# Optimization experiments

Hardware: AMD Instinct MI355X
Metric: run time of the kernel (lower is better)

The kernel has to match this reference:

```python
import jax, jax.numpy as jnp
import numpy as np

N = 50000      # num nodes
C_IN = 128     # channels[0]
C_OUT = 128    # channels[1]
D = 16         # fixed node degree
T = 4          # diffusion steps
H_MLP = 64     # diff_mlp hidden
H_GRU = 128    # GRUAggr hidden
EPS = 0.01


def setup_inputs() -> dict:
    key = jax.random.key(0)
    ks = jax.random.split(key, 10)
    node_attr = jax.random.normal(ks[0], (N, C_IN), jnp.float32)
    # adjacency sorted by source: node i owns columns [i*D, i*D+D)
    src = jnp.repeat(jnp.arange(N), D)
    dst = jax.random.randint(ks[1], (N * D,), 0, N)
    edge_index = jnp.stack([src, dst])                       # [2, N*D]
    slices = jnp.stack([jnp.arange(N) * D, jnp.full((N,), D)], axis=1)  # [N,2] (start,count)
    noise = EPS * jax.random.normal(ks[2], (T, N, D), jnp.float32)      # eps*randn per step
    init = lambda k, shape, fan: (jax.random.normal(k, shape, jnp.float32) / np.sqrt(fan))
    W1 = init(ks[3], ((1 + T) * C_IN, H_MLP), (1 + T) * C_IN)
    b1 = jnp.zeros((H_MLP,), jnp.float32)
    W2 = init(ks[4], (H_MLP, 1), H_MLP)
    b2 = jnp.zeros((1,), jnp.float32)
    Wx = init(ks[5], (C_IN, 3 * H_GRU), C_IN)
    Wh = init(ks[6], (H_GRU, 3 * H_GRU), H_GRU)
    bx = jnp.zeros((3 * H_GRU,), jnp.float32)
    bh = jnp.zeros((3 * H_GRU,), jnp.float32)
    Wo = init(ks[7], (H_GRU, C_OUT), H_GRU)
    bo = jnp.zeros((C_OUT,), jnp.float32)
    return dict(node_attr=node_attr, edge_index=edge_index, slices=slices, noise=noise,
                W1=W1, b1=b1, W2=W2, b2=b2, Wx=Wx, Wh=Wh, bx=bx, bh=bh, Wo=Wo, bo=bo)


def _gru(x_seq, Wx, Wh, bx, bh):
    # x_seq: [T+1, N, C]; torch GRU gate order (r, z, n)
    H = Wh.shape[0]
    def step(h, x):
        gx = x @ Wx + bx
        gh = h @ Wh + bh
        xr, xz, xn = jnp.split(gx, 3, axis=-1)
        hr, hz, hn = jnp.split(gh, 3, axis=-1)
        r = jax.nn.sigmoid(xr + hr)
        z = jax.nn.sigmoid(xz + hz)
        n = jnp.tanh(xn + r * hn)
        return (1.0 - z) * n + z * h, None
    h0 = jnp.zeros((x_seq.shape[1], H), x_seq.dtype)
    h, _ = jax.lax.scan(step, h0, x_seq)
    return h


def reference(node_attr, edge_index, slices, noise, W1, b1, W2, b2, Wx, Wh, bx, bh, Wo, bo):
    n, C = node_attr.shape
    t_steps, _, deg = noise.shape
    dst = edge_index[1]
    walk_embeds = jnp.zeros((n, 1 + t_steps, C), node_attr.dtype).at[:, 0, :].set(node_attr)
    cur = jnp.arange(n)
    for t in range(t_steps):
        starts = slices[cur, 0]                              # slice_cat(adj, adj_slic_t)
        nbr = dst[starts[:, None] + jnp.arange(deg)]         # [N, D] neighbor node ids
        v_t = node_attr[nbr]                                 # [N, D, C]
        # diff_mlp on [prefix walk embed | candidate neighbor]: split the first
        # linear layer so the shared prefix is computed once per node (position
        # 1+t of walk_embeds is still zero, matching the original fill order).
        h_pre = walk_embeds.reshape(n, (1 + t_steps) * C) @ W1 + b1       # [N, H_MLP]
        h_nbr = jnp.einsum('ndc,ch->ndh', v_t, W1[(1 + t) * C:(2 + t) * C])
        logp = (jax.nn.relu(h_pre[:, None, :] + h_nbr) @ W2)[..., 0] + b2[0]  # [N, D]
        logp = jax.lax.stop_gradient(logp)                   # torch.no_grad()
        # scatter_logsumexp over init node == logsumexp over the D candidates
        p = jnp.exp(logp - jax.nn.logsumexp(logp, axis=1, keepdims=True)) + noise[t]
        sel = jnp.argmax(p, axis=1)                          # scatter_max per init node
        cur = nbr[jnp.arange(n), sel]                        # walks_t
        walk_embeds = walk_embeds.at[:, 1 + t, :].set(node_attr[cur])
    h = _gru(jnp.transpose(walk_embeds, (1, 0, 2)), Wx, Wh, bx, bh)
    return h @ Wo + bo                                       # [N, C_OUT]
```

## Files before the change

kernel.cpp:

```cpp
#include <hip/hip_runtime.h>
#include <math.h>

#define NND 50000
#define DEG 16

typedef __attribute__((ext_vector_type(8))) short short8v;
typedef __attribute__((ext_vector_type(4))) float float4v;

#define OFF_HPRE 0ULL
#define OFF_PROJ 12800000ULL
#define OFF_XB   64000000ULL
#define OFF_IDX  102400000ULL
#define OFF_BQF  103600384ULL
#define OFF_WOF  103862528ULL
#define WS_NEED  103895296ULL

#define LOG2E 1.44269504088896f

__device__ __forceinline__ float fast_sig(float x){
    return __builtin_amdgcn_rcpf(1.f + __builtin_amdgcn_exp2f(-LOG2E*x));
}
__device__ __forceinline__ float fast_tanh(float x){
    return fmaf(-2.f, __builtin_amdgcn_rcpf(1.f + __builtin_amdgcn_exp2f((2.f*LOG2E)*x)), 1.f);
}
__device__ __forceinline__ unsigned short f2bf(float f){
    unsigned int u = __float_as_uint(f);
    u += 0x7FFFu + ((u >> 16) & 1u);
    return (unsigned short)(u >> 16);
}
__device__ __forceinline__ float bf2f(unsigned short h){
    return __uint_as_float(((unsigned int)h) << 16);
}

__global__ __launch_bounds__(256) void k_iota(int* __restrict__ idx0){
    int i = blockIdx.x*256 + threadIdx.x;
    if (i < NND) idx0[i] = i;
}

__global__ __launch_bounds__(256) void k_projall(const float* __restrict__ A,
    const float* __restrict__ W1, const float* __restrict__ b1,
    float* __restrict__ hpre, float* __restrict__ proj)
{
    __shared__ float Al[64][33];
    __shared__ float Bl[32][68];
    const int tid = threadIdx.x;
    const int row0 = blockIdx.x << 6;
    const int y = blockIdx.y;
    const float* B = W1 + (size_t)y*128*64;
    const int row_t = tid >> 4, col_t = tid & 15;
    float4 acc[4];
#pragma unroll
    for (int i=0;i<4;i++) acc[i] = make_float4(0.f,0.f,0.f,0.f);
    for (int k0 = 0; k0 < 128; k0 += 32){
#pragma unroll
        for (int r=0;r<2;r++){
            int am = (tid>>3) + (r<<5);
            int ak = (tid&7) << 2;
            int gr = row0 + am; if (gr >= NND) gr = NND-1;
            float4 v = *(const float4*)(A + (size_t)gr*128 + k0 + ak);
            Al[am][ak] = v.x; Al[am][ak+1] = v.y; Al[am][ak+2] = v.z; Al[am][ak+3] = v.w;
        }
#pragma unroll
        for (int r=0;r<2;r++){
            int p = (r<<8) + tid;
            int bk = p >> 4, bc = (p & 15) << 2;
            *(float4*)(&Bl[bk][bc]) = *(const float4*)(B + (size_t)(k0+bk)*64 + bc);
        }
        __syncthreads();
#pragma unroll 8
        for (int k=0;k<32;k++){
            float4 b = *(const float4*)(&Bl[k][col_t<<2]);
#pragma unroll
            for (int i=0;i<4;i++){
                float a = Al[(row_t<<2)+i][k];
                acc[i].x = fmaf(a, b.x, acc[i].x);
                acc[i].y = fmaf(a, b.y, acc[i].y);
                acc[i].z = fmaf(a, b.z, acc[i].z);
                acc[i].w = fmaf(a, b.w, acc[i].w);
            }
        }
        __syncthreads();
    }
    float4 bb = make_float4(0.f,0.f,0.f,0.f);
    if (y == 0) bb = *(const float4*)(b1 + (col_t<<2));
    float* dst = (y == 0) ? hpre : (proj + (size_t)(y-1)*NND*64);
#pragma unroll
    for (int i=0;i<4;i++){
        int gr = row0 + (row_t<<2) + i;
        if (gr < NND){
            float4 o = make_float4(acc[i].x+bb.x, acc[i].y+bb.y, acc[i].z+bb.z, acc[i].w+bb.w);
            *(float4*)(dst + (size_t)gr*64 + (col_t<<2)) = o;
        }
    }
}

__global__ __launch_bounds__(256) void k_walk4(
    const float* __restrict__ hpre0, const float* __restrict__ proj,
    const int* __restrict__ dst, const float* __restrict__ W2,
    const float* __restrict__ b2, const float* __restrict__ noise,
    int* __restrict__ idxb)
{
    const int tid = threadIdx.x;
    const int sg = tid >> 4, l = tid & 15;
    const int gi = (blockIdx.x << 4) + sg;
    float4 hp = *(const float4*)(hpre0 + ((size_t)gi<<6) + (l<<2));
    float4 w2 = *(const float4*)(W2 + (l<<2));
    const float b2s = b2[0];
    int curv = gi;
#pragma unroll 1
    for (int t=0; t<4; t++){
        const float* pj = proj + (size_t)t*NND*64;
        const int nbr = dst[curv*DEG + l];
        float4 val[16];
#pragma unroll
        for (int d=0; d<16; d++){
            int nd = __shfl(nbr, d, 16);
            val[d] = *(const float4*)(pj + ((size_t)nd<<6) + (l<<2));
        }
        float lp = 0.f;
#pragma unroll
        for (int d=0; d<16; d++){
            float4 v = val[d];
            float q =  fmaxf(hp.x+v.x,0.f)*w2.x;
            q = fmaf(fmaxf(hp.y+v.y,0.f), w2.y, q);
            q = fmaf(fmaxf(hp.z+v.z,0.f), w2.z, q);
            q = fmaf(fmaxf(hp.w+v.w,0.f), w2.w, q);
            q += __shfl_xor(q, 1, 16);
            q += __shfl_xor(q, 2, 16);
            q += __shfl_xor(q, 4, 16);
            q += __shfl_xor(q, 8, 16);
            if (l == d) lp = q + b2s;
        }
        float mx = lp;
#pragma unroll
        for (int off=8; off; off>>=1) mx = fmaxf(mx, __shfl_xor(mx, off, 16));
        float s = expf(lp - mx);
#pragma unroll
        for (int off=8; off; off>>=1) s += __shfl_xor(s, off, 16);
        float p = expf(lp - mx - logf(s)) + noise[(size_t)t*NND*DEG + ((size_t)gi<<4) + l];
        float bv = p; int bi = l;
#pragma unroll
        for (int off=8; off; off>>=1){
            float ov = __shfl_xor(bv, off, 16);
            int   oi = __shfl_xor(bi, off, 16);
            if (ov > bv || (ov == bv && oi < bi)){ bv = ov; bi = oi; }
        }
        int sel = __shfl(nbr, bi, 16);
        if (l == 0) idxb[(size_t)(t+1)*NND + gi] = sel;
        float4 u = *(const float4*)(pj + ((size_t)sel<<6) + (l<<2));
        hp.x += u.x; hp.y += u.y; hp.z += u.z; hp.w += u.w;
        curv = sel;
    }
}

__global__ __launch_bounds__(256) void k_pack_x(const float* __restrict__ na,
    unsigned short* __restrict__ Xb)
{
    int i = blockIdx.x*256 + threadIdx.x;
    if (i < NND*32){
        float4 v = *(const float4*)(na + (size_t)i*4);
        unsigned long long pk = (unsigned long long)f2bf(v.x)
            | ((unsigned long long)f2bf(v.y) << 16)
            | ((unsigned long long)f2bf(v.z) << 32)
            | ((unsigned long long)f2bf(v.w) << 48);
        *(unsigned long long*)(Xb + (size_t)i*4) = pk;
    }
}

__global__ __launch_bounds__(256) void k_pack_bqf(const float* __restrict__ Wx,
    const float* __restrict__ Wh, unsigned short* __restrict__ BqF)
{
    int i = blockIdx.x*256 + threadIdx.x;
    int jj = i & 7, lane = (i>>3)&63, ct = (i>>9)&7, c = (i>>12)&7, y = i>>15;
    int g = ct>>1, jh = ct&1, mm = lane&15, quad = lane>>4;
    int jg = (y<<5) + (jh<<4) + mm;
    int k = (c<<5) + (quad<<3) + jj;
    float v = 0.f;
    if (k < 128){
        if (g < 3) v = Wh[k*384 + g*128 + jg];
    } else {
        int kk = k - 128;
        if (g == 0)      v = Wx[kk*384 + jg];
        else if (g == 1) v = Wx[kk*384 + 128 + jg];
        else if (g == 3) v = Wx[kk*384 + 256 + jg];
    }
    BqF[i] = f2bf(v);
}

__global__ __launch_bounds__(256) void k_pack_wof(const float* __restrict__ Wo,
    unsigned short* __restrict__ WoF)
{
    int i = blockIdx.x*256 + threadIdx.x;
    int jj = i & 7, lane = (i>>3)&63, ct = (i>>9)&7, c = i>>12;
    int n = (ct<<4) + (lane&15);
    int k = (c<<5) + ((lane>>4)<<3) + jj;
    WoF[i] = f2bf(Wo[k*128 + n]);
}

__global__ __launch_bounds__(256,2) void k_gru5(
    const unsigned short* __restrict__ Xb,
    const unsigned short* __restrict__ BqF,
    const unsigned short* __restrict__ WoF,
    const float* __restrict__ bx, const float* __restrict__ bh,
    const float* __restrict__ bo, const int* __restrict__ idxb,
    float* __restrict__ out)
{
    __shared__ unsigned short A_l[8192];
    __shared__ unsigned short X_l[16384];
    const int tid = threadIdx.x;
    const int w = tid >> 6, lane = tid & 63;
    const int m = lane & 15, quad = lane >> 4;
    const int row0 = blockIdx.x << 6;
    const int r = tid & 63, q = tid >> 6;
    int gr = row0 + r; if (gr >= NND) gr = NND-1;
    const int rt_s = r >> 4, m_s = r & 15;
    float brr[2], bzz[2], bxn[2], bhn[2];
#pragma unroll
    for (int jh=0; jh<2; jh++){
        int j = (w<<5) + (jh<<4) + m;
        brr[jh] = bx[j] + bh[j];
        bzz[jh] = bx[128+j] + bh[128+j];
        bxn[jh] = bx[256+j];
        bhn[jh] = bh[256+j];
    }
    unsigned short holdv[2][4][4];
    short8v xv[4];
    {
        const int xr = idxb[gr];
        const unsigned short* xrow = Xb + (size_t)xr*128 + (q<<5);
#pragma unroll
        for (int u=0;u<4;u++) xv[u] = *(const short8v*)(xrow + (u<<3));
#pragma unroll
        for (int u=0;u<4;u++)
            *(short8v*)(X_l + (((rt_s<<2)+q)*64 + (u<<4) + m_s)*8) = xv[u];
        const int xr1 = idxb[NND + gr];
        const unsigned short* xrow1 = Xb + (size_t)xr1*128 + (q<<5);
#pragma unroll
        for (int u=0;u<4;u++) xv[u] = *(const short8v*)(xrow1 + (u<<3));
    }
    __syncthreads();

#pragma unroll 1
    for (int s=0; s<5; s++){
        const unsigned short* Xcur = X_l + ((s&1)<<13);
        float4v zero = {0.f,0.f,0.f,0.f};
        float4v acc[32];
#pragma unroll
        for (int i=0;i<32;i++) acc[i] = zero;
        const int c0 = (s == 0) ? 4 : 0;
        for (int c=c0;c<8;c++){
            const unsigned short* asrc = (c < 4) ? A_l : Xcur;
            short8v afr[4];
#pragma unroll
            for (int rt=0;rt<4;rt++)
                afr[rt] = *(const short8v*)(asrc + (((rt<<2) + (c&3))*64 + lane)*8);
            const unsigned short* bp = BqF + ((((size_t)w*8 + c)*8)*64 + lane)*8;
#pragma unroll
            for (int ct=0;ct<8;ct++){
                short8v bf = *(const short8v*)(bp + (ct<<9));
#pragma unroll
                for (int rt=0;rt<4;rt++)
                    acc[(ct<<2)+rt] = __builtin_amdgcn_mfma_f32_16x16x32_bf16(afr[rt], bf, acc[(ct<<2)+rt], 0,0,0);
            }
        }
        if (s < 4){
            unsigned short* Xnxt = X_l + (((s+1)&1)<<13);
#pragma unroll
            for (int u=0;u<4;u++)
                *(short8v*)(Xnxt + (((rt_s<<2)+q)*64 + (u<<4) + m_s)*8) = xv[u];
            if (s < 3){
                const int xr = idxb[(size_t)(s+2)*NND + gr];
                const unsigned short* xrow = Xb + (size_t)xr*128 + (q<<5);
#pragma unroll
                for (int u=0;u<4;u++) xv[u] = *(const short8v*)(xrow + (u<<3));
            }
        }
#pragma unroll
        for (int jh=0; jh<2; jh++){
#pragma unroll
            for (int rt=0; rt<4; rt++){
#pragma unroll
                for (int r4=0; r4<4; r4++){
                    float rg = fast_sig(acc[(jh<<2)+rt][r4] + brr[jh]);
                    float zg = fast_sig(acc[((2+jh)<<2)+rt][r4] + bzz[jh]);
                    float ng = fast_tanh(acc[((6+jh)<<2)+rt][r4] + bxn[jh] + rg*(acc[((4+jh)<<2)+rt][r4] + bhn[jh]));
                    float hold = (s == 0) ? 0.f : bf2f(holdv[jh][rt][r4]);
                    holdv[jh][rt][r4] = f2bf((1.f - zg)*ng + zg*hold);
                }
            }
        }
        __syncthreads();
#pragma unroll
        for (int jh=0; jh<2; jh++)
#pragma unroll
            for (int rt=0; rt<4; rt++)
#pragma unroll
                for (int r4=0; r4<4; r4++){
                    int ha = ((((rt<<2)+w)*64 + (((jh<<1)+(m>>3))<<4) + (quad<<2)+r4)<<3) + (m&7);
                    A_l[ha] = holdv[jh][rt][r4];
                }
        __syncthreads();
    }
    float4v zero = {0.f,0.f,0.f,0.f};
    float4v acco[8];
#pragma unroll
    for (int i=0;i<8;i++) acco[i] = zero;
    for (int c=0;c<4;c++){
        short8v afr[4];
#pragma unroll
        for (int rt=0;rt<4;rt++)
            afr[rt] = *(const short8v*)(A_l + (((rt<<2) + c)*64 + lane)*8);
#pragma unroll
        for (int cto=0;cto<2;cto++){
            short8v bf = *(const short8v*)(WoF + (((size_t)(c*8 + (w<<1)+cto))*64 + lane)*8);
#pragma unroll
            for (int rt=0;rt<4;rt++)
                acco[(cto<<2)+rt] = __builtin_amdgcn_mfma_f32_16x16x32_bf16(afr[rt], bf, acco[(cto<<2)+rt], 0,0,0);
        }
    }
#pragma unroll
    for (int cto=0; cto<2; cto++){
        int col = (w<<5) + (cto<<4) + m;
        float bb = bo[col];
#pragma unroll
        for (int rt=0; rt<4; rt++){
#pragma unroll
            for (int r4=0; r4<4; r4++){
                int row = row0 + (rt<<4) + (quad<<2) + r4;
                if (row < NND) out[(size_t)row*128 + col] = acco[(cto<<2)+rt][r4] + bb;
            }
        }
    }
}

extern "C" void kernel_launch(void* const* d_in, const int* in_sizes, int n_in,
                              void* d_out, int out_size, void* d_ws, size_t ws_size,
                              hipStream_t stream)
{
    const float* node_attr = (const float*)d_in[0];
    const int*   edge_index= (const int*)  d_in[1];
    const float* noise = (const float*)d_in[3];
    const float* W1 = (const float*)d_in[4];
    const float* b1 = (const float*)d_in[5];
    const float* W2 = (const float*)d_in[6];
    const float* b2 = (const float*)d_in[7];
    const float* Wx = (const float*)d_in[8];
    const float* Wh = (const float*)d_in[9];
    const float* bx = (const float*)d_in[10];
    const float* bh = (const float*)d_in[11];
    const float* Wo = (const float*)d_in[12];
    const float* bo = (const float*)d_in[13];
    const int* dst = edge_index + (size_t)NND*DEG;
    float* out = (float*)d_out;
    if (ws_size < WS_NEED) return;

    char* ws = (char*)d_ws;
    float* hpre = (float*)(ws + OFF_HPRE);
    float* proj = (float*)(ws + OFF_PROJ);
    unsigned short* Xb  = (unsigned short*)(ws + OFF_XB);
    int* idxb = (int*)(ws + OFF_IDX);
    unsigned short* BqF = (unsigned short*)(ws + OFF_BQF);
    unsigned short* WoF = (unsigned short*)(ws + OFF_WOF);

    k_iota<<<dim3(196), dim3(256), 0, stream>>>(idxb);
    k_pack_x  <<<dim3(6250), dim3(256), 0, stream>>>(node_attr, Xb);
    k_pack_bqf<<<dim3(512),  dim3(256), 0, stream>>>(Wx, Wh, BqF);
    k_pack_wof<<<dim3(64),   dim3(256), 0, stream>>>(Wo, WoF);

    k_projall<<<dim3(782, 5), dim3(256), 0, stream>>>(node_attr, W1, b1, hpre, proj);
    k_walk4<<<dim3(3125), dim3(256), 0, stream>>>(hpre, proj, dst, W2, b2, noise, idxb);

    k_gru5<<<dim3(782), dim3(256), 0, stream>>>(Xb, BqF, WoF, bx, bh, bo, idxb, out);
}
```

Before: 386.2 us.

## Fuse setup packing kernels, single-buffer GRU X tile, skip zero-weight MFMAs

```diff
diff --git a/kernel.cpp b/kernel.cpp
--- a/kernel.cpp
+++ b/kernel.cpp
@@ -32,12 +32,48 @@
     return __uint_as_float(((unsigned int)h) << 16);
 }
 
-__global__ __launch_bounds__(256) void k_iota(int* __restrict__ idx0){
+__global__ __launch_bounds__(256) void k_setup(const float* __restrict__ na,
+    unsigned short* __restrict__ Xb,
+    const float* __restrict__ Wx, const float* __restrict__ Wh,
+    unsigned short* __restrict__ BqF,
+    const float* __restrict__ Wo, unsigned short* __restrict__ WoF,
+    int* __restrict__ idx0)
+{
     int i = blockIdx.x*256 + threadIdx.x;
+    if (i < NND*32){
+        float4 v = *(const float4*)(na + (size_t)i*4);
+        unsigned long long pk = (unsigned long long)f2bf(v.x)
+            | ((unsigned long long)f2bf(v.y) << 16)
+            | ((unsigned long long)f2bf(v.z) << 32)
+            | ((unsigned long long)f2bf(v.w) << 48);
+        *(unsigned long long*)(Xb + (size_t)i*4) = pk;
+    }
+    if (i < 131072){
+        int jj = i & 7, lane = (i>>3)&63, ct = (i>>9)&7, c = (i>>12)&7, y = i>>15;
+        int g = ct>>1, jh = ct&1, mm = lane&15, quad = lane>>4;
+        int jg = (y<<5) + (jh<<4) + mm;
+        int k = (c<<5) + (quad<<3) + jj;
+        float v = 0.f;
+        if (k < 128){
+            if (g < 3) v = Wh[k*384 + g*128 + jg];
+        } else {
+            int kk = k - 128;
+            if (g == 0)      v = Wx[kk*384 + jg];
+            else if (g == 1) v = Wx[kk*384 + 128 + jg];
+            else if (g == 3) v = Wx[kk*384 + 256 + jg];
+        }
+        BqF[i] = f2bf(v);
+    }
+    if (i < 16384){
+        int jj = i & 7, lane = (i>>3)&63, ct = (i>>9)&7, c = i>>12;
+        int n = (ct<<4) + (lane&15);
+        int k = (c<<5) + ((lane>>4)<<3) + jj;
+        WoF[i] = f2bf(Wo[k*128 + n]);
+    }
     if (i < NND) idx0[i] = i;
 }
 
-__global__ __launch_bounds__(256) void k_projall(const float* __restrict__ A,
+__global__ __launch_bounds__(256,4) void k_projall(const float* __restrict__ A,
     const float* __restrict__ W1, const float* __restrict__ b1,
     float* __restrict__ hpre, float* __restrict__ proj)
 {
@@ -153,51 +189,7 @@
     }
 }
 
-__global__ __launch_bounds__(256) void k_pack_x(const float* __restrict__ na,
-    unsigned short* __restrict__ Xb)
-{
-    int i = blockIdx.x*256 + threadIdx.x;
-    if (i < NND*32){
-        float4 v = *(const float4*)(na + (size_t)i*4);
-        unsigned long long pk = (unsigned long long)f2bf(v.x)
-            | ((unsigned long long)f2bf(v.y) << 16)
-            | ((unsigned long long)f2bf(v.z) << 32)
-            | ((unsigned long long)f2bf(v.w) << 48);
-        *(unsigned long long*)(Xb + (size_t)i*4) = pk;
-    }
-}
-
-__global__ __launch_bounds__(256) void k_pack_bqf(const float* __restrict__ Wx,
-    const float* __restrict__ Wh, unsigned short* __restrict__ BqF)
-{
-    int i = blockIdx.x*256 + threadIdx.x;
-    int jj = i & 7, lane = (i>>3)&63, ct = (i>>9)&7, c = (i>>12)&7, y = i>>15;
-    int g = ct>>1, jh = ct&1, mm = lane&15, quad = lane>>4;
-    int jg = (y<<5) + (jh<<4) + mm;
-    int k = (c<<5) + (quad<<3) + jj;
-    float v = 0.f;
-    if (k < 128){
-        if (g < 3) v = Wh[k*384 + g*128 + jg];
-    } else {
-        int kk = k - 128;
-        if (g == 0)      v = Wx[kk*384 + jg];
-        else if (g == 1) v = Wx[kk*384 + 128 + jg];
-        else if (g == 3) v = Wx[kk*384 + 256 + jg];
-    }
-    BqF[i] = f2bf(v);
-}
-
-__global__ __launch_bounds__(256) void k_pack_wof(const float* __restrict__ Wo,
-    unsigned short* __restrict__ WoF)
-{
-    int i = blockIdx.x*256 + threadIdx.x;
-    int jj = i & 7, lane = (i>>3)&63, ct = (i>>9)&7, c = i>>12;
-    int n = (ct<<4) + (lane&15);
-    int k = (c<<5) + ((lane>>4)<<3) + jj;
-    WoF[i] = f2bf(Wo[k*128 + n]);
-}
-
-__global__ __launch_bounds__(256,2) void k_gru5(
+__global__ __launch_bounds__(256,4) void k_gru5(
     const unsigned short* __restrict__ Xb,
     const unsigned short* __restrict__ BqF,
     const unsigned short* __restrict__ WoF,
@@ -206,7 +198,7 @@
     float* __restrict__ out)
 {
     __shared__ unsigned short A_l[8192];
-    __shared__ unsigned short X_l[16384];
+    __shared__ unsigned short X_l[8192];
     const int tid = threadIdx.x;
     const int w = tid >> 6, lane = tid & 63;
     const int m = lane & 15, quad = lane >> 4;
@@ -242,37 +234,25 @@
 
 #pragma unroll 1
     for (int s=0; s<5; s++){
-        const unsigned short* Xcur = X_l + ((s&1)<<13);
         float4v zero = {0.f,0.f,0.f,0.f};
         float4v acc[32];
 #pragma unroll
         for (int i=0;i<32;i++) acc[i] = zero;
         const int c0 = (s == 0) ? 4 : 0;
         for (int c=c0;c<8;c++){
-            const unsigned short* asrc = (c < 4) ? A_l : Xcur;
+            const unsigned short* asrc = (c < 4) ? A_l : X_l;
             short8v afr[4];
 #pragma unroll
             for (int rt=0;rt<4;rt++)
                 afr[rt] = *(const short8v*)(asrc + (((rt<<2) + (c&3))*64 + lane)*8);
             const unsigned short* bp = BqF + ((((size_t)w*8 + c)*8)*64 + lane)*8;
 #pragma unroll
-            for (int ct=0;ct<8;ct++){
+            for (int ci=0;ci<6;ci++){
+                int ct = (ci < 4) ? ci : ((c < 4) ? ci : ci + 2);
                 short8v bf = *(const short8v*)(bp + (ct<<9));
 #pragma unroll
                 for (int rt=0;rt<4;rt++)
                     acc[(ct<<2)+rt] = __builtin_amdgcn_mfma_f32_16x16x32_bf16(afr[rt], bf, acc[(ct<<2)+rt], 0,0,0);
-            }
-        }
-        if (s < 4){
-            unsigned short* Xnxt = X_l + (((s+1)&1)<<13);
-#pragma unroll
-            for (int u=0;u<4;u++)
-                *(short8v*)(Xnxt + (((rt_s<<2)+q)*64 + (u<<4) + m_s)*8) = xv[u];
-            if (s < 3){
-                const int xr = idxb[(size_t)(s+2)*NND + gr];
-                const unsigned short* xrow = Xb + (size_t)xr*128 + (q<<5);
-#pragma unroll
-                for (int u=0;u<4;u++) xv[u] = *(const short8v*)(xrow + (u<<3));
             }
         }
 #pragma unroll
@@ -299,6 +279,17 @@
                     int ha = ((((rt<<2)+w)*64 + (((jh<<1)+(m>>3))<<4) + (quad<<2)+r4)<<3) + (m&7);
                     A_l[ha] = holdv[jh][rt][r4];
                 }
+        if (s < 4){
+#pragma unroll
+            for (int u=0;u<4;u++)
+                *(short8v*)(X_l + (((rt_s<<2)+q)*64 + (u<<4) + m_s)*8) = xv[u];
+            if (s < 3){
+                const int xr = idxb[(size_t)(s+2)*NND + gr];
+                const unsigned short* xrow = Xb + (size_t)xr*128 + (q<<5);
+#pragma unroll
+                for (int u=0;u<4;u++) xv[u] = *(const short8v*)(xrow + (u<<3));
+            }
+        }
         __syncthreads();
     }
     float4v zero = {0.f,0.f,0.f,0.f};
@@ -362,10 +353,7 @@
     unsigned short* BqF = (unsigned short*)(ws + OFF_BQF);
     unsigned short* WoF = (unsigned short*)(ws + OFF_WOF);
 
-    k_iota<<<dim3(196), dim3(256), 0, stream>>>(idxb);
-    k_pack_x  <<<dim3(6250), dim3(256), 0, stream>>>(node_attr, Xb);
-    k_pack_bqf<<<dim3(512),  dim3(256), 0, stream>>>(Wx, Wh, BqF);
-    k_pack_wof<<<dim3(64),   dim3(256), 0, stream>>>(Wo, WoF);
+    k_setup<<<dim3(6250), dim3(256), 0, stream>>>(node_attr, Xb, Wx, Wh, BqF, Wo, WoF, idxb);
 
     k_projall<<<dim3(782, 5), dim3(256), 0, stream>>>(node_attr, W1, b1, hpre, proj);
     k_walk4<<<dim3(3125), dim3(256), 0, stream>>>(hpre, proj, dst, W2, b2, noise, idxb);
```

After: 775.4 us. 101% more time.
